# Kernel tuning notes

Measured on AMD Instinct MI355X. Metric: run time of the kernel, lower is better.

The kernel has to match this reference:

```python
import jax, jax.numpy as jnp
import numpy as np

N, E, G = 100000, 1600000, 64   # nodes, edges, graphs
IN, H, OUT = 32, 128, 3


def setup_inputs() -> dict:
    key = jax.random.key(0)
    ks = jax.random.split(key, 24)
    def w(k, i, o):
        return (jax.random.normal(k, (i, o), jnp.float32) / np.sqrt(i)).astype(jnp.float32)
    inp = {
        "x": jax.random.normal(ks[0], (N, IN), jnp.float32),
        "edge_index": jax.random.randint(ks[1], (2, E), 0, N, dtype=jnp.int32).astype(jnp.int64),
        "batch": jnp.sort(jax.random.randint(ks[2], (N,), 0, G, dtype=jnp.int32)).astype(jnp.int64),
        # SAGEConv layer 0 (in->hidden): lin_l (neighbors, with bias), lin_r (root, no bias)
        "Wl0": w(ks[3], IN, H), "bl0": jnp.zeros((H,), jnp.float32), "Wr0": w(ks[4], IN, H),
        # SAGEConv layers 1,2 (hidden->hidden)
        "Wl1": w(ks[5], H, H), "bl1": jnp.zeros((H,), jnp.float32), "Wr1": w(ks[6], H, H),
        "Wl2": w(ks[7], H, H), "bl2": jnp.zeros((H,), jnp.float32), "Wr2": w(ks[8], H, H),
        # output head
        "Wfc": w(ks[9], H, OUT), "bfc": jnp.zeros((OUT,), jnp.float32),
        # aux MLP on (dim1, dim3)
        "Wa1": w(ks[10], 2, H), "ba1": jnp.zeros((H,), jnp.float32),
        "Wa2": w(ks[11], H, H), "ba2": jnp.zeros((H,), jnp.float32),
        "Wao": w(ks[12], H, 1), "bao": jnp.zeros((1,), jnp.float32),
    }
    return inp


def _sage_conv(x, src, dst, Wl, bl, Wr):
    # PyG SAGEConv (mean aggr): out = lin_l(mean_{j in N(i)} x_j) + lin_r(x_i)
    msg = x[src]                                   # [E, d] gather
    agg = jax.ops.segment_sum(msg, dst, num_segments=N)
    cnt = jax.ops.segment_sum(jnp.ones((src.shape[0],), x.dtype), dst, num_segments=N)
    mean = agg / jnp.maximum(cnt, 1.0)[:, None]
    return mean @ Wl + bl + x @ Wr


def reference(x, edge_index, batch,
              Wl0, bl0, Wr0, Wl1, bl1, Wr1, Wl2, bl2, Wr2,
              Wfc, bfc, Wa1, ba1, Wa2, ba2, Wao, bao):
    src, dst = edge_index[0], edge_index[1]
    h = jax.nn.relu(_sage_conv(x, src, dst, Wl0, bl0, Wr0))   # dropout is identity in eval
    h = jax.nn.relu(_sage_conv(h, src, dst, Wl1, bl1, Wr1))
    h = jax.nn.relu(_sage_conv(h, src, dst, Wl2, bl2, Wr2))
    main = h @ Wfc + bfc                                      # [N, 3]
    dim1, dim3 = main[:, 0], main[:, 2]
    aux_in = jnp.stack([dim1, dim3], axis=-1)                 # [N, 2]
    a = jax.nn.relu(aux_in @ Wa1 + ba1)
    a = jax.nn.relu(a @ Wa2 + ba2)
    aux_out = (a @ Wao + bao)[:, 0]                           # [N]
    final = jnp.stack([dim1, aux_out, dim3], axis=-1)         # [N, 3]
    # global mean pool over graph ids
    s = jax.ops.segment_sum(final, batch, num_segments=G)
    c = jax.ops.segment_sum(jnp.ones((final.shape[0],), final.dtype), batch, num_segments=G)
    return s / jnp.maximum(c, 1.0)[:, None]                   # [G, 3]
```

## Files before the change

### kernel.cpp

```cpp
#include <hip/hip_runtime.h>

#define NR 128
#define PART_CH 4096
typedef unsigned short ushortT;
typedef __attribute__((ext_vector_type(8))) short short8;
typedef __attribute__((ext_vector_type(4))) float float4v;
typedef __attribute__((ext_vector_type(2))) float float2v;

__device__ __forceinline__ unsigned short f32_to_bf16_rne(float f) {
    unsigned u = __float_as_uint(f);
    unsigned r = (u + 0x7fffu + ((u >> 16) & 1u)) >> 16;
    return (unsigned short)r;
}

__device__ __forceinline__ unsigned char f32_to_fp8(float f) {
    return (unsigned char)(__builtin_amdgcn_cvt_pk_fp8_f32(f, f, 0, false) & 0xff);
}

__device__ __forceinline__ void accum8(float* acc, uint4 v) {
    unsigned u[4] = {v.x, v.y, v.z, v.w};
#pragma unroll
    for (int q = 0; q < 4; q++) {
        acc[2 * q]     += __uint_as_float(u[q] << 16);
        acc[2 * q + 1] += __uint_as_float(u[q] & 0xffff0000u);
    }
}

__device__ __forceinline__ void accum16_fp8(float* ag, uint4 v) {
    unsigned w[4] = {v.x, v.y, v.z, v.w};
#pragma unroll
    for (int m = 0; m < 4; m++) {
        float2v lo = __builtin_amdgcn_cvt_pk_f32_fp8(w[m], false);
        float2v hi = __builtin_amdgcn_cvt_pk_f32_fp8(w[m], true);
        ag[4 * m + 0] += lo.x;
        ag[4 * m + 1] += lo.y;
        ag[4 * m + 2] += hi.x;
        ag[4 * m + 3] += hi.y;
    }
}


__launch_bounds__(256)
__global__ void bucket_count(const int* __restrict__ dst, int* __restrict__ bcnt, int E, int NB) {
    __shared__ int h[1024];
    int t = threadIdx.x;
    for (int j = t; j < NB; j += 256) h[j] = 0;
    __syncthreads();
    int e0 = blockIdx.x * PART_CH;
    int e1 = min(e0 + PART_CH, E);
    for (int base = e0; base < e1; base += 2048) {
        int idx = base + t;
        int d[8];
        int cnt = 0;
#pragma unroll
        for (int u = 0; u < 8; u++) {
            int e = idx + u * 256;
            if (e < e1) d[cnt++] = dst[e];
        }
        for (int u = 0; u < cnt; u++) atomicAdd(&h[d[u] >> 7], 1);
    }
    __syncthreads();
    for (int j = t; j < NB; j += 256) {
        int v = h[j];
        if (v) atomicAdd(&bcnt[j], v);
    }
}

__launch_bounds__(256)
__global__ void bucket_scan(const int* __restrict__ bcnt, int* __restrict__ bstart,
                            int* __restrict__ gcur, int NB, int E) {
    __shared__ int sh[256];
    int t = threadIdx.x;
    int v[4];
    int tot = 0;
#pragma unroll
    for (int j = 0; j < 4; j++) {
        int idx = t * 4 + j;
        v[j] = (idx < NB) ? bcnt[idx] : 0;
        tot += v[j];
    }
    sh[t] = tot;
    __syncthreads();
    for (int off = 1; off < 256; off <<= 1) {
        int add = (t >= off) ? sh[t - off] : 0;
        __syncthreads();
        sh[t] += add;
        __syncthreads();
    }
    int run = sh[t] - tot;
#pragma unroll
    for (int j = 0; j < 4; j++) {
        int idx = t * 4 + j;
        if (idx < NB) { bstart[idx] = run; gcur[idx] = run; }
        run += v[j];
    }
    if (t == 0) bstart[NB] = E;
}

__launch_bounds__(256)
__global__ void partition_edges(const int* __restrict__ src, const int* __restrict__ dst,
                                int* __restrict__ gcur, unsigned* __restrict__ packed,
                                int E, int NB) {
    __shared__ int hist[1024];
    __shared__ int base[1024];
    int t = threadIdx.x;
    int e0 = blockIdx.x * PART_CH;
    int e1 = min(e0 + PART_CH, E);
    for (int j = t; j < NB; j += 256) hist[j] = 0;
    __syncthreads();
    for (int bb = e0; bb < e1; bb += 2048) {
        int idx = bb + t;
        int d[8];
        int cnt = 0;
#pragma unroll
        for (int u = 0; u < 8; u++) {
            int e = idx + u * 256;
            if (e < e1) d[cnt++] = dst[e];
        }
        for (int u = 0; u < cnt; u++) atomicAdd(&hist[d[u] >> 7], 1);
    }
    __syncthreads();
    for (int j = t; j < NB; j += 256) {
        int h = hist[j];
        base[j] = h ? atomicAdd(&gcur[j], h) : 0;
    }
    __syncthreads();
    for (int j = t; j < NB; j += 256) hist[j] = base[j];
    __syncthreads();
    for (int bb = e0; bb < e1; bb += 2048) {
        int idx = bb + t;
        int d[8], s[8];
        int cnt = 0;
#pragma unroll
        for (int u = 0; u < 8; u++) {
            int e = idx + u * 256;
            if (e < e1) { d[cnt] = dst[e]; s[cnt] = src[e]; cnt++; }
        }
        for (int u = 0; u < cnt; u++) {
            int dd = d[u];
            int pos = atomicAdd(&hist[dd >> 7], 1);
            packed[pos] = (unsigned)s[u] | ((unsigned)(dd & (NR - 1)) << 17);
        }
    }
}

__launch_bounds__(256)
__global__ void bucket_sort(const unsigned* __restrict__ packed, const int* __restrict__ bstart,
                            int* __restrict__ row_start, int* __restrict__ srcs, int N) {
    __shared__ int cnt[NR];
    __shared__ int sc[NR];
    __shared__ int cur[NR];
    int b = blockIdx.x, t = threadIdx.x;
    int nb0 = b * NR;
    int nnode = min(NR, N - nb0);
    int lo = bstart[b], hi = bstart[b + 1];
    if (t < NR) cnt[t] = 0;
    __syncthreads();
    for (int bb = lo; bb < hi; bb += 2048) {
        int idx = bb + t;
        unsigned pk[8];
        int c = 0;
#pragma unroll
        for (int u = 0; u < 8; u++) {
            int e = idx + u * 256;
            if (e < hi) pk[c++] = packed[e];
        }
        for (int u = 0; u < c; u++) atomicAdd(&cnt[pk[u] >> 17], 1);
    }
    __syncthreads();
    if (t < NR) sc[t] = cnt[t];
    __syncthreads();
    for (int off = 1; off < NR; off <<= 1) {
        int add = (t >= off && t < NR) ? sc[t - off] : 0;
        __syncthreads();
        if (t < NR) sc[t] += add;
        __syncthreads();
    }
    if (t < nnode) {
        int s = lo + sc[t] - cnt[t];
        row_start[nb0 + t] = s;
        cur[t] = s;
    }
    if (t == 0 && nb0 + nnode == N) row_start[N] = hi;
    __syncthreads();
    for (int bb = lo; bb < hi; bb += 2048) {
        int idx = bb + t;
        unsigned pk[8];
        int c = 0;
#pragma unroll
        for (int u = 0; u < 8; u++) {
            int e = idx + u * 256;
            if (e < hi) pk[c++] = packed[e];
        }
        for (int u = 0; u < c; u++) {
            int pos = atomicAdd(&cur[pk[u] >> 17], 1);
            srcs[pos] = (int)(pk[u] & 0x1FFFFu);
        }
    }
}


__global__ void prep_fused(const float* __restrict__ x, ushortT* __restrict__ xbf, int n4,
                           const float* __restrict__ Wl0, const float* __restrict__ Wr0,
                           const float* __restrict__ Wl1, const float* __restrict__ Wr1,
                           const float* __restrict__ Wl2, const float* __restrict__ Wr2,
                           const float* __restrict__ Wa2,
                           ushortT* __restrict__ Wt0, ushortT* __restrict__ Wt1,
                           ushortT* __restrict__ Wt2, ushortT* __restrict__ Wa2t) {
    int tid0 = blockIdx.x * 256 + threadIdx.x;
    if (tid0 < n4) {
        float4 v = ((const float4*)x)[tid0];
        ushort4 o;
        o.x = f32_to_bf16_rne(v.x);
        o.y = f32_to_bf16_rne(v.y);
        o.z = f32_to_bf16_rne(v.z);
        o.w = f32_to_bf16_rne(v.w);
        ((ushort4*)xbf)[tid0] = o;
        return;
    }
    int tid = tid0 - n4;
    if (tid < 8192) {
        int col = tid >> 6, k = tid & 63;
        float v = (k < 32) ? Wl0[k * 128 + col] : Wr0[(k - 32) * 128 + col];
        Wt0[col * 64 + ((k + 8 * col) & 63)] = f32_to_bf16_rne(v);
    } else if (tid < 8192 + 32768) {
        int j = tid - 8192;
        int col = j >> 8, k = j & 255;
        float v = (k < 128) ? Wl1[k * 128 + col] : Wr1[(k - 128) * 128 + col];
        Wt1[(k >> 6) * 8192 + col * 64 + (((k & 63) + 8 * col) & 63)] = f32_to_bf16_rne(v);
    } else if (tid < 8192 + 65536) {
        int j = tid - 8192 - 32768;
        int col = j >> 8, k = j & 255;
        float v = (k < 128) ? Wl2[k * 128 + col] : Wr2[(k - 128) * 128 + col];
        Wt2[(k >> 6) * 8192 + col * 64 + (((k & 63) + 8 * col) & 63)] = f32_to_bf16_rne(v);
    } else if (tid < 8192 + 65536 + 16384) {
        int j = tid - 8192 - 65536;
        int col = j >> 7, k = j & 127;
        Wa2t[(k >> 6) * 8192 + col * 64 + (((k & 63) + 8 * col) & 63)] = f32_to_bf16_rne(Wa2[k * 128 + col]);
    }
}


__launch_bounds__(256)
__global__ void agg_fp8(const uint4* __restrict__ hp, const int* __restrict__ srcs,
                        const int* __restrict__ rs, ushortT* __restrict__ amb, int n) {
    int tid = blockIdx.x * 256 + threadIdx.x;
    if (tid >= n * 8) return;
    int i = tid >> 3, c = tid & 7;
    int lo = rs[i], hi = rs[i + 1];
    float ag[16];
#pragma unroll
    for (int j = 0; j < 16; j++) ag[j] = 0.f;
    int e = lo;
    for (; e + 8 <= hi; e += 8) {
        int s[8];
#pragma unroll
        for (int u = 0; u < 8; u++) s[u] = srcs[e + u];
        uint4 v[8];
#pragma unroll
        for (int u = 0; u < 8; u++) v[u] = hp[(size_t)s[u] * 8 + c];
#pragma unroll
        for (int u = 0; u < 8; u++) accum16_fp8(ag, v[u]);
    }
    for (; e < hi; ++e) accum16_fp8(ag, hp[(size_t)srcs[e] * 8 + c]);
    float inv = 1.0f / (float)max(hi - lo, 1);
    uint4 o0, o1;
    o0.x = (unsigned)f32_to_bf16_rne(ag[0] * inv)  | ((unsigned)f32_to_bf16_rne(ag[1] * inv) << 16);
    o0.y = (unsigned)f32_to_bf16_rne(ag[2] * inv)  | ((unsigned)f32_to_bf16_rne(ag[3] * inv) << 16);
    o0.z = (unsigned)f32_to_bf16_rne(ag[4] * inv)  | ((unsigned)f32_to_bf16_rne(ag[5] * inv) << 16);
    o0.w = (unsigned)f32_to_bf16_rne(ag[6] * inv)  | ((unsigned)f32_to_bf16_rne(ag[7] * inv) << 16);
    o1.x = (unsigned)f32_to_bf16_rne(ag[8] * inv)  | ((unsigned)f32_to_bf16_rne(ag[9] * inv) << 16);
    o1.y = (unsigned)f32_to_bf16_rne(ag[10] * inv) | ((unsigned)f32_to_bf16_rne(ag[11] * inv) << 16);
    o1.z = (unsigned)f32_to_bf16_rne(ag[12] * inv) | ((unsigned)f32_to_bf16_rne(ag[13] * inv) << 16);
    o1.w = (unsigned)f32_to_bf16_rne(ag[14] * inv) | ((unsigned)f32_to_bf16_rne(ag[15] * inv) << 16);
    ((uint4*)amb)[(size_t)i * 16 + c * 2]     = o0;
    ((uint4*)amb)[(size_t)i * 16 + c * 2 + 1] = o1;
}

__launch_bounds__(256)
__global__ void agg_bf16(const uint4* __restrict__ xp, const int* __restrict__ srcs,
                         const int* __restrict__ rs, ushortT* __restrict__ amb, int n) {
    int tid = blockIdx.x * 256 + threadIdx.x;
    if (tid >= n * 4) return;
    int i = tid >> 2, c = tid & 3;
    int lo = rs[i], hi = rs[i + 1];
    float ag[8];
#pragma unroll
    for (int j = 0; j < 8; j++) ag[j] = 0.f;
    int e = lo;
    for (; e + 8 <= hi; e += 8) {
        int s[8];
#pragma unroll
        for (int u = 0; u < 8; u++) s[u] = srcs[e + u];
        uint4 v[8];
#pragma unroll
        for (int u = 0; u < 8; u++) v[u] = xp[(size_t)s[u] * 4 + c];
#pragma unroll
        for (int u = 0; u < 8; u++) accum8(ag, v[u]);
    }
    for (; e < hi; ++e) accum8(ag, xp[(size_t)srcs[e] * 4 + c]);
    float inv = 1.0f / (float)max(hi - lo, 1);
    uint4 o;
    o.x = (unsigned)f32_to_bf16_rne(ag[0] * inv) | ((unsigned)f32_to_bf16_rne(ag[1] * inv) << 16);
    o.y = (unsigned)f32_to_bf16_rne(ag[2] * inv) | ((unsigned)f32_to_bf16_rne(ag[3] * inv) << 16);
    o.z = (unsigned)f32_to_bf16_rne(ag[4] * inv) | ((unsigned)f32_to_bf16_rne(ag[5] * inv) << 16);
    o.w = (unsigned)f32_to_bf16_rne(ag[6] * inv) | ((unsigned)f32_to_bf16_rne(ag[7] * inv) << 16);
    ((uint4*)amb)[(size_t)i * 4 + c] = o;
}


__device__ __forceinline__ void stage_copy(ushortT* sW, const ushortT* Wq, int t) {
    const uint4* Wg = (const uint4*)Wq;
    uint4* Ws = (uint4*)sW;
#pragma unroll
    for (int j = 0; j < 4; j++) Ws[t + j * 256] = Wg[t + j * 256];
}

template <int KH>
__device__ __forceinline__ void gemm_body(
        const ushortT* __restrict__ Amb, const ushortT* __restrict__ Ah,
        const ushortT* __restrict__ Wt, const float* __restrict__ bias,
        ushortT* __restrict__ outbf, unsigned char* __restrict__ outf8, int n) {
    constexpr int NKS = KH / 32;
    __shared__ __attribute__((aligned(16))) ushortT sW[128 * 64];
    int t = threadIdx.x;
    stage_copy(sW, Wt, t);
    int wv = t >> 6, lane = t & 63;
    int q = lane >> 4, cid = lane & 15;
    int row = blockIdx.x * 64 + wv * 16 + cid;
    int rc = min(row, n - 1);

    short8 am[NKS], ah[NKS];
    if constexpr (KH == 32) {
        am[0] = *(const short8*)(Amb + (size_t)rc * 32 + q * 8);
        ah[0] = *(const short8*)(Ah + (size_t)rc * 32 + q * 8);
    } else {
#pragma unroll
        for (int ks = 0; ks < NKS; ks++) {
            am[ks] = *(const short8*)(Amb + (size_t)rc * 128 + q * 32 + ks * 8);
            ah[ks] = *(const short8*)(Ah + (size_t)rc * 128 + ks * 32 + q * 8);
        }
    }
    __syncthreads();

    float4v acc[8];
#pragma unroll
    for (int j = 0; j < 8; j++) acc[j] = (float4v){0.f, 0.f, 0.f, 0.f};
    int pbase = q * 8 + 8 * cid;
    if constexpr (KH == 32) {
        {
            int p = pbase & 63;
#pragma unroll
            for (int j = 0; j < 8; ++j) {
                short8 b = *(const short8*)(sW + (j * 16 + cid) * 64 + p);
                acc[j] = __builtin_amdgcn_mfma_f32_16x16x32_bf16(am[0], b, acc[j], 0, 0, 0);
            }
        }
        {
            int p = (32 + pbase) & 63;
#pragma unroll
            for (int j = 0; j < 8; ++j) {
                short8 b = *(const short8*)(sW + (j * 16 + cid) * 64 + p);
                acc[j] = __builtin_amdgcn_mfma_f32_16x16x32_bf16(ah[0], b, acc[j], 0, 0, 0);
            }
        }
    } else {
#pragma unroll
        for (int st = 0; st < 4; st++) {
            if (st > 0) {
                __syncthreads();
                stage_copy(sW, Wt + st * 8192, t);
                __syncthreads();
            }
#pragma unroll
            for (int ksl = 0; ksl < 2; ksl++) {
                short8 a = (st < 2) ? am[st * 2 + ksl] : ah[(st - 2) * 2 + ksl];
                int p = (ksl * 32 + pbase) & 63;
#pragma unroll
                for (int j = 0; j < 8; ++j) {
                    short8 b = *(const short8*)(sW + (j * 16 + cid) * 64 + p);
                    acc[j] = __builtin_amdgcn_mfma_f32_16x16x32_bf16(a, b, acc[j], 0, 0, 0);
                }
            }
        }
    }
    float bo[8];
#pragma unroll
    for (int j = 0; j < 8; ++j) bo[j] = bias[j * 16 + cid];
    int orow = blockIdx.x * 64 + wv * 16 + q * 4;
#pragma unroll
    for (int rr = 0; rr < 4; ++rr) {
        int r = orow + rr;
        if (r < n) {
#pragma unroll
            for (int j = 0; j < 8; ++j) {
                int col = j * 16 + cid;
                float v = fmaxf(acc[j][rr] + bo[j], 0.f);
                outbf[(size_t)r * 128 + col] = f32_to_bf16_rne(v);
                int pc = ((col >> 3) & 3) * 32 + ((col >> 5) << 3) + (col & 7);
                outf8[(size_t)r * 128 + pc] = f32_to_fp8(v);
            }
        }
    }
}

__launch_bounds__(256, 2)
__global__ void gemm32(const ushortT* __restrict__ Amb, const ushortT* __restrict__ Ah,
                       const ushortT* __restrict__ Wt, const float* __restrict__ bias,
                       ushortT* __restrict__ outbf, unsigned char* __restrict__ outf8, int n) {
    gemm_body<32>(Amb, Ah, Wt, bias, outbf, outf8, n);
}

__launch_bounds__(256, 2)
__global__ void gemm128(const ushortT* __restrict__ Amb, const ushortT* __restrict__ Ah,
                        const ushortT* __restrict__ Wt, const float* __restrict__ bias,
                        ushortT* __restrict__ outbf, unsigned char* __restrict__ outf8, int n) {
    gemm_body<128>(Amb, Ah, Wt, bias, outbf, outf8, n);
}


__launch_bounds__(256, 2)
__global__ void gemm_fin(const ushortT* __restrict__ Amb, const ushortT* __restrict__ Ah,
                         const ushortT* __restrict__ Wt, const float* __restrict__ bias,
                         const float* __restrict__ Wfc, const float* __restrict__ bfc,
                         const ushortT* __restrict__ Wa2t, const float* __restrict__ Wa1,
                         const float* __restrict__ ba1, const float* __restrict__ ba2,
                         const float* __restrict__ Wao, const float* __restrict__ bao,
                         float* __restrict__ fin, int n) {
    __shared__ __attribute__((aligned(16))) ushortT sW[128 * 64];
    __shared__ float sD1[64], sD3[64];
    __shared__ float sWa1a[128], sWa1b[128], sBa1[128];
    int t = threadIdx.x;
    stage_copy(sW, Wt, t);
    if (t < 128) { sWa1a[t] = Wa1[t]; sWa1b[t] = Wa1[128 + t]; sBa1[t] = ba1[t]; }
    int wv = t >> 6, lane = t & 63;
    int q = lane >> 4, cid = lane & 15;
    int row = blockIdx.x * 64 + wv * 16 + cid;
    int rc = min(row, n - 1);

    short8 am[4], ah[4];
#pragma unroll
    for (int ks = 0; ks < 4; ks++) {
        am[ks] = *(const short8*)(Amb + (size_t)rc * 128 + q * 32 + ks * 8);
        ah[ks] = *(const short8*)(Ah + (size_t)rc * 128 + ks * 32 + q * 8);
    }
    __syncthreads();

    float4v acc[8];
#pragma unroll
    for (int j = 0; j < 8; j++) acc[j] = (float4v){0.f, 0.f, 0.f, 0.f};
    int pbase = q * 8 + 8 * cid;
#pragma unroll
    for (int st = 0; st < 4; st++) {
        if (st > 0) {
            __syncthreads();
            stage_copy(sW, Wt + st * 8192, t);
            __syncthreads();
        }
#pragma unroll
        for (int ksl = 0; ksl < 2; ksl++) {
            short8 a = (st < 2) ? am[st * 2 + ksl] : ah[(st - 2) * 2 + ksl];
            int p = (ksl * 32 + pbase) & 63;
#pragma unroll
            for (int j = 0; j < 8; ++j) {
                short8 b = *(const short8*)(sW + (j * 16 + cid) * 64 + p);
                acc[j] = __builtin_amdgcn_mfma_f32_16x16x32_bf16(a, b, acc[j], 0, 0, 0);
            }
        }
    }

    float bo[8], w1[8], w3[8];
#pragma unroll
    for (int j = 0; j < 8; ++j) {
        int col = j * 16 + cid;
        bo[j] = bias[col];
        w1[j] = Wfc[col * 3 + 0];
        w3[j] = Wfc[col * 3 + 2];
    }
    float bfc0 = bfc[0], bfc2 = bfc[2];
#pragma unroll
    for (int rr = 0; rr < 4; ++rr) {
        float p1 = 0.f, p3 = 0.f;
#pragma unroll
        for (int j = 0; j < 8; ++j) {
            float v = fmaxf(acc[j][rr] + bo[j], 0.f);
            p1 += v * w1[j];
            p3 += v * w3[j];
        }
        p1 += __shfl_xor(p1, 1, 64); p3 += __shfl_xor(p3, 1, 64);
        p1 += __shfl_xor(p1, 2, 64); p3 += __shfl_xor(p3, 2, 64);
        p1 += __shfl_xor(p1, 4, 64); p3 += __shfl_xor(p3, 4, 64);
        p1 += __shfl_xor(p1, 8, 64); p3 += __shfl_xor(p3, 8, 64);
        if (cid == 0) {
            int rowl = wv * 16 + q * 4 + rr;
            float d1 = p1 + bfc0, d3 = p3 + bfc2;
            sD1[rowl] = d1;
            sD3[rowl] = d3;
            int r = blockIdx.x * 64 + rowl;
            if (r < n) {
                fin[(size_t)r * 3 + 0] = d1;
                fin[(size_t)r * 3 + 2] = d3;
            }
        }
    }
    __syncthreads();

    int rl = wv * 16 + cid;
    float d1a = sD1[rl], d3a = sD3[rl];
    float4v hacc[8];
#pragma unroll
    for (int j = 0; j < 8; j++) hacc[j] = (float4v){0.f, 0.f, 0.f, 0.f};
#pragma unroll
    for (int hs = 0; hs < 2; hs++) {
        if (hs > 0) __syncthreads();
        stage_copy(sW, Wa2t + hs * 8192, t);
        __syncthreads();
#pragma unroll
        for (int ksl = 0; ksl < 2; ++ksl) {
            int k0 = hs * 64 + ksl * 32 + q * 8;
            short8 a0;
#pragma unroll
            for (int j = 0; j < 8; ++j) {
                int k = k0 + j;
                float v0 = fmaxf(fmaf(d1a, sWa1a[k], fmaf(d3a, sWa1b[k], sBa1[k])), 0.f);
                a0[j] = (short)f32_to_bf16_rne(v0);
            }
            int p = (ksl * 32 + pbase) & 63;
#pragma unroll
            for (int j = 0; j < 8; ++j) {
                short8 b = *(const short8*)(sW + (j * 16 + cid) * 64 + p);
                hacc[j] = __builtin_amdgcn_mfma_f32_16x16x32_bf16(a0, b, hacc[j], 0, 0, 0);
            }
        }
    }
    float b2[8], wo[8];
#pragma unroll
    for (int j = 0; j < 8; ++j) {
        int col = j * 16 + cid;
        b2[j] = ba2[col];
        wo[j] = Wao[col];
    }
    float bao0 = bao[0];
#pragma unroll
    for (int rr = 0; rr < 4; ++rr) {
        float s = 0.f;
#pragma unroll
        for (int j = 0; j < 8; ++j) s += fmaxf(hacc[j][rr] + b2[j], 0.f) * wo[j];
        s += __shfl_xor(s, 1, 64);
        s += __shfl_xor(s, 2, 64);
        s += __shfl_xor(s, 4, 64);
        s += __shfl_xor(s, 8, 64);
        int r = blockIdx.x * 64 + wv * 16 + q * 4 + rr;
        if (cid == 0 && r < n) fin[(size_t)r * 3 + 1] = s + bao0;
    }
}


__global__ void pool_kernel(const float* __restrict__ fin, const int* __restrict__ batch,
                            float* __restrict__ out, int n) {
    int g = blockIdx.x, t = threadIdx.x;
    int lo = 0, hi = n;
    while (lo < hi) { int mid = (lo + hi) >> 1; if (batch[mid] < g) lo = mid + 1; else hi = mid; }
    int start = lo;
    lo = 0; hi = n;
    while (lo < hi) { int mid = (lo + hi) >> 1; if (batch[mid] < g + 1) lo = mid + 1; else hi = mid; }
    int end = lo;
    float s0 = 0.f, s1 = 0.f, s2 = 0.f;
    for (int i = start + t; i < end; i += 256) {
        s0 += fin[(size_t)i * 3 + 0];
        s1 += fin[(size_t)i * 3 + 1];
        s2 += fin[(size_t)i * 3 + 2];
    }
    __shared__ float r0[256], r1[256], r2[256];
    r0[t] = s0; r1[t] = s1; r2[t] = s2;
    __syncthreads();
    for (int off = 128; off > 0; off >>= 1) {
        if (t < off) { r0[t] += r0[t + off]; r1[t] += r1[t + off]; r2[t] += r2[t + off]; }
        __syncthreads();
    }
    if (t == 0) {
        float c = (float)max(end - start, 1);
        out[g * 3 + 0] = r0[0] / c;
        out[g * 3 + 1] = r1[0] / c;
        out[g * 3 + 2] = r2[0] / c;
    }
}


extern "C" void kernel_launch(void* const* d_in, const int* in_sizes, int n_in,
                              void* d_out, int out_size, void* d_ws, size_t ws_size,
                              hipStream_t stream) {
    const float* x    = (const float*)d_in[0];
    const int*   ei   = (const int*)d_in[1];
    const int*   batch= (const int*)d_in[2];
    const float* Wl0  = (const float*)d_in[3];
    const float* bl0  = (const float*)d_in[4];
    const float* Wr0  = (const float*)d_in[5];
    const float* Wl1  = (const float*)d_in[6];
    const float* bl1  = (const float*)d_in[7];
    const float* Wr1  = (const float*)d_in[8];
    const float* Wl2  = (const float*)d_in[9];
    const float* bl2  = (const float*)d_in[10];
    const float* Wr2  = (const float*)d_in[11];
    const float* Wfc  = (const float*)d_in[12];
    const float* bfc  = (const float*)d_in[13];
    const float* Wa1  = (const float*)d_in[14];
    const float* ba1  = (const float*)d_in[15];
    const float* Wa2  = (const float*)d_in[16];
    const float* ba2  = (const float*)d_in[17];
    const float* Wao  = (const float*)d_in[18];
    const float* bao  = (const float*)d_in[19];

    const int N = in_sizes[0] / 32;
    const int E = in_sizes[1] / 2;
    const int G = out_size / 3;
    const int* src = ei;
    const int* dst = ei + E;
    float* out = (float*)d_out;
    const int NB = (N + NR - 1) / NR;

    char* p = (char*)d_ws;
    auto carve = [&](size_t bytes) {
        void* r = (void*)p;
        p += (bytes + 255) & ~(size_t)255;
        return r;
    };
    int*           bcnt     = (int*)carve((size_t)NB * 4);
    int*           bstart   = (int*)carve((size_t)(NB + 1) * 4);
    int*           gcur     = (int*)carve((size_t)NB * 4);
    int*           row_start= (int*)carve((size_t)(N + 1) * 4);
    unsigned*      packed   = (unsigned*)carve((size_t)E * 4);
    int*           srcs     = (int*)carve((size_t)E * 4);
    ushortT*       xbf      = (ushortT*)carve((size_t)N * 32 * 2);
    ushortT*       hbf0     = (ushortT*)carve((size_t)N * 128 * 2);
    ushortT*       hbf1     = (ushortT*)carve((size_t)N * 128 * 2);
    unsigned char* hf8_0    = (unsigned char*)carve((size_t)N * 128);
    unsigned char* hf8_1    = (unsigned char*)carve((size_t)N * 128);
    ushortT*       amb0     = (ushortT*)carve((size_t)N * 32 * 2);
    ushortT*       amb1     = (ushortT*)carve((size_t)N * 128 * 2);
    ushortT*       amb2     = (ushortT*)carve((size_t)N * 128 * 2);
    float*         fin      = (float*)carve((size_t)N * 3 * 4);
    ushortT*       Wt0      = (ushortT*)carve((size_t)128 * 64 * 2);
    ushortT*       Wt1      = (ushortT*)carve((size_t)128 * 256 * 2);
    ushortT*       Wt2      = (ushortT*)carve((size_t)128 * 256 * 2);
    ushortT*       Wa2t     = (ushortT*)carve((size_t)128 * 128 * 2);

    const int gemm_grid = (N + 63) / 64;
    const int part_grid = (E + PART_CH - 1) / PART_CH;
    const int n4 = N * 32 / 4;

    prep_fused<<<(n4 + 90112 + 255) / 256, 256, 0, stream>>>(
        x, xbf, n4, Wl0, Wr0, Wl1, Wr1, Wl2, Wr2, Wa2, Wt0, Wt1, Wt2, Wa2t);

    hipMemsetAsync(bcnt, 0, (size_t)NB * 4, stream);
    bucket_count<<<part_grid, 256, 0, stream>>>(dst, bcnt, E, NB);
    bucket_scan<<<1, 256, 0, stream>>>(bcnt, bstart, gcur, NB, E);
    partition_edges<<<part_grid, 256, 0, stream>>>(src, dst, gcur, packed, E, NB);
    bucket_sort<<<NB, 256, 0, stream>>>(packed, bstart, row_start, srcs, N);

    agg_bf16<<<(N * 4 + 255) / 256, 256, 0, stream>>>(
        (const uint4*)xbf, srcs, row_start, amb0, N);
    gemm32<<<gemm_grid, 256, 0, stream>>>(amb0, xbf, Wt0, bl0, hbf0, hf8_0, N);
    agg_fp8<<<(N * 8 + 255) / 256, 256, 0, stream>>>(
        (const uint4*)hf8_0, srcs, row_start, amb1, N);
    gemm128<<<gemm_grid, 256, 0, stream>>>(amb1, hbf0, Wt1, bl1, hbf1, hf8_1, N);
    agg_fp8<<<(N * 8 + 255) / 256, 256, 0, stream>>>(
        (const uint4*)hf8_1, srcs, row_start, amb2, N);
    gemm_fin<<<gemm_grid, 256, 0, stream>>>(
        amb2, hbf1, Wt2, bl2, Wfc, bfc, Wa2t, Wa1, ba1, ba2, Wao, bao, fin, N);

    pool_kernel<<<G, 256, 0, stream>>>(fin, batch, out, N);
}
```

Before: 354.5 us.

## Store gather sources as per-chunk planes and split aggregation grid by chunk

Feature tables used by the neighbor aggregation are now stored in a planar layout: each 16-byte chunk column is its own contiguous plane. The prep kernel and the GEMM epilogue write this layout. Aggregation blocks are assigned one chunk per block, so each block gathers only from a compact plane of N*16 bytes, which should improve cache locality for the random gathers. The cost is an extra planar copy of x and a strided scatter in the GEMM epilogue. Each thread also re-reads row_start and srcs for its own chunk, so the index loads are no longer shared across the 4 or 8 threads that previously covered a row.

```diff
diff --git a/kernel.cpp b/kernel.cpp
--- a/kernel.cpp
+++ b/kernel.cpp
@@ -200,7 +200,8 @@
 }
 
 
-__global__ void prep_fused(const float* __restrict__ x, ushortT* __restrict__ xbf, int n4,
+__global__ void prep_fused(const float* __restrict__ x, ushortT* __restrict__ xbf,
+                           ushortT* __restrict__ xplan, int n4,
                            const float* __restrict__ Wl0, const float* __restrict__ Wr0,
                            const float* __restrict__ Wl1, const float* __restrict__ Wr1,
                            const float* __restrict__ Wl2, const float* __restrict__ Wr2,
@@ -216,6 +217,9 @@
         o.z = f32_to_bf16_rne(v.z);
         o.w = f32_to_bf16_rne(v.w);
         ((ushort4*)xbf)[tid0] = o;
+        int i = tid0 >> 3, j = tid0 & 7;
+        int Nn = n4 >> 3;
+        ((ushort4*)xplan)[((size_t)(j >> 1) * Nn + i) * 2 + (j & 1)] = o;
         return;
     }
     int tid = tid0 - n4;
@@ -244,9 +248,10 @@
 __launch_bounds__(256)
 __global__ void agg_fp8(const uint4* __restrict__ hp, const int* __restrict__ srcs,
                         const int* __restrict__ rs, ushortT* __restrict__ amb, int n) {
-    int tid = blockIdx.x * 256 + threadIdx.x;
-    if (tid >= n * 8) return;
-    int i = tid >> 3, c = tid & 7;
+    int c = blockIdx.x & 7;
+    int i = (blockIdx.x >> 3) * 256 + threadIdx.x;
+    if (i >= n) return;
+    const uint4* plane = hp + (size_t)c * n;
     int lo = rs[i], hi = rs[i + 1];
     float ag[16];
 #pragma unroll
@@ -258,11 +263,11 @@
         for (int u = 0; u < 8; u++) s[u] = srcs[e + u];
         uint4 v[8];
 #pragma unroll
-        for (int u = 0; u < 8; u++) v[u] = hp[(size_t)s[u] * 8 + c];
+        for (int u = 0; u < 8; u++) v[u] = plane[s[u]];
 #pragma unroll
         for (int u = 0; u < 8; u++) accum16_fp8(ag, v[u]);
     }
-    for (; e < hi; ++e) accum16_fp8(ag, hp[(size_t)srcs[e] * 8 + c]);
+    for (; e < hi; ++e) accum16_fp8(ag, plane[srcs[e]]);
     float inv = 1.0f / (float)max(hi - lo, 1);
     uint4 o0, o1;
     o0.x = (unsigned)f32_to_bf16_rne(ag[0] * inv)  | ((unsigned)f32_to_bf16_rne(ag[1] * inv) << 16);
@@ -280,9 +285,10 @@
 __launch_bounds__(256)
 __global__ void agg_bf16(const uint4* __restrict__ xp, const int* __restrict__ srcs,
                          const int* __restrict__ rs, ushortT* __restrict__ amb, int n) {
-    int tid = blockIdx.x * 256 + threadIdx.x;
-    if (tid >= n * 4) return;
-    int i = tid >> 2, c = tid & 3;
+    int c = blockIdx.x & 3;
+    int i = (blockIdx.x >> 2) * 256 + threadIdx.x;
+    if (i >= n) return;
+    const uint4* plane = xp + (size_t)c * n;
     int lo = rs[i], hi = rs[i + 1];
     float ag[8];
 #pragma unroll
@@ -294,11 +300,11 @@
         for (int u = 0; u < 8; u++) s[u] = srcs[e + u];
         uint4 v[8];
 #pragma unroll
-        for (int u = 0; u < 8; u++) v[u] = xp[(size_t)s[u] * 4 + c];
+        for (int u = 0; u < 8; u++) v[u] = plane[s[u]];
 #pragma unroll
         for (int u = 0; u < 8; u++) accum8(ag, v[u]);
     }
-    for (; e < hi; ++e) accum8(ag, xp[(size_t)srcs[e] * 4 + c]);
+    for (; e < hi; ++e) accum8(ag, plane[srcs[e]]);
     float inv = 1.0f / (float)max(hi - lo, 1);
     uint4 o;
     o.x = (unsigned)f32_to_bf16_rne(ag[0] * inv) | ((unsigned)f32_to_bf16_rne(ag[1] * inv) << 16);
@@ -387,6 +393,7 @@
     float bo[8];
 #pragma unroll
     for (int j = 0; j < 8; ++j) bo[j] = bias[j * 16 + cid];
+    size_t pstride = (size_t)n * 16;
     int orow = blockIdx.x * 64 + wv * 16 + q * 4;
 #pragma unroll
     for (int rr = 0; rr < 4; ++rr) {
@@ -398,7 +405,7 @@
                 float v = fmaxf(acc[j][rr] + bo[j], 0.f);
                 outbf[(size_t)r * 128 + col] = f32_to_bf16_rne(v);
                 int pc = ((col >> 3) & 3) * 32 + ((col >> 5) << 3) + (col & 7);
-                outf8[(size_t)r * 128 + pc] = f32_to_fp8(v);
+                outf8[(size_t)(pc >> 4) * pstride + (size_t)r * 16 + (pc & 15)] = f32_to_fp8(v);
             }
         }
     }
@@ -632,6 +639,7 @@
     unsigned*      packed   = (unsigned*)carve((size_t)E * 4);
     int*           srcs     = (int*)carve((size_t)E * 4);
     ushortT*       xbf      = (ushortT*)carve((size_t)N * 32 * 2);
+    ushortT*       xplan    = (ushortT*)carve((size_t)N * 32 * 2);
     ushortT*       hbf0     = (ushortT*)carve((size_t)N * 128 * 2);
     ushortT*       hbf1     = (ushortT*)carve((size_t)N * 128 * 2);
     unsigned char* hf8_0    = (unsigned char*)carve((size_t)N * 128);
@@ -647,10 +655,11 @@
 
     const int gemm_grid = (N + 63) / 64;
     const int part_grid = (E + PART_CH - 1) / PART_CH;
-    const int n4 = N * 32 / 4;
+    const int n4 = N * 8;
+    const int rowblk = (N + 255) / 256;
 
     prep_fused<<<(n4 + 90112 + 255) / 256, 256, 0, stream>>>(
-        x, xbf, n4, Wl0, Wr0, Wl1, Wr1, Wl2, Wr2, Wa2, Wt0, Wt1, Wt2, Wa2t);
+        x, xbf, xplan, n4, Wl0, Wr0, Wl1, Wr1, Wl2, Wr2, Wa2, Wt0, Wt1, Wt2, Wa2t);
 
     hipMemsetAsync(bcnt, 0, (size_t)NB * 4, stream);
     bucket_count<<<part_grid, 256, 0, stream>>>(dst, bcnt, E, NB);
@@ -658,13 +667,13 @@
     partition_edges<<<part_grid, 256, 0, stream>>>(src, dst, gcur, packed, E, NB);
     bucket_sort<<<NB, 256, 0, stream>>>(packed, bstart, row_start, srcs, N);
 
-    agg_bf16<<<(N * 4 + 255) / 256, 256, 0, stream>>>(
-        (const uint4*)xbf, srcs, row_start, amb0, N);
+    agg_bf16<<<rowblk * 4, 256, 0, stream>>>(
+        (const uint4*)xplan, srcs, row_start, amb0, N);
     gemm32<<<gemm_grid, 256, 0, stream>>>(amb0, xbf, Wt0, bl0, hbf0, hf8_0, N);
-    agg_fp8<<<(N * 8 + 255) / 256, 256, 0, stream>>>(
+    agg_fp8<<<rowblk * 8, 256, 0, stream>>>(
         (const uint4*)hf8_0, srcs, row_start, amb1, N);
     gemm128<<<gemm_grid, 256, 0, stream>>>(amb1, hbf0, Wt1, bl1, hbf1, hf8_1, N);
-    agg_fp8<<<(N * 8 + 255) / 256, 256, 0, stream>>>(
+    agg_fp8<<<rowblk * 8, 256, 0, stream>>>(
         (const uint4*)hf8_1, srcs, row_start, amb2, N);
     gemm_fin<<<gemm_grid, 256, 0, stream>>>(
         amb2, hbf1, Wt2, bl2, Wfc, bfc, Wa2t, Wa1, ba1, ba2, Wao, bao, fin, N);
```

After: 439.9 us. 24.1% more time.
